# Performance work log

Hardware: AMD Instinct MI355X
Metric: run time of the kernel (lower is better)

Reference implementation:

```python
import jax, jax.numpy as jnp
import numpy as np

NUM_HEADS = 16
EPS = 1e-6
ROPE_BASE = 10000.0

def _thw(N, TT):
    table = {2640: (3, 22, 40), 1530: (3, 17, 30), 6120: (3, 34, 60), 660: (3, 11, 20)}
    return table.get(N - TT, (3, 23, 40))

def _positions(t, h, w):
    tt, hh, ww = np.meshgrid(np.arange(t), np.arange(h), np.arange(w), indexing='ij')
    return jnp.asarray(np.stack([tt, hh, ww], -1).reshape(-1, 3), jnp.float32)  # (THW, 3)

def _rope1d(x, pos):
    # x: (B,H,T,d) one axis-chunk, pos: (T,) positions for that axis
    d = x.shape[-1]
    inv_freq = 1.0 / (ROPE_BASE ** (jnp.arange(0, d, 2, dtype=jnp.float32) / d))
    ang = pos[:, None] * inv_freq                     # (T, d/2)
    cos = jnp.concatenate([jnp.cos(ang)] * 2, -1)     # (T, d)
    sin = jnp.concatenate([jnp.sin(ang)] * 2, -1)
    x1, x2 = x[..., : d // 2], x[..., d // 2:]
    return x * cos + jnp.concatenate([-x2, x1], -1) * sin

def _rope3d(x, pos, TT):
    # first TT tokens (text) pass through; video tokens get per-axis rotation
    pre, vid = x[:, :, :TT], x[:, :, TT:]
    chunks = jnp.split(vid, 3, axis=-1)               # t/h/w axis chunks
    rot = [_rope1d(c, pos[:, i]) for i, c in enumerate(chunks)]
    return jnp.concatenate([pre, jnp.concatenate(rot, -1)], axis=2)

def _rms(x, w):
    return x * jax.lax.rsqrt(jnp.mean(x * x, -1, keepdims=True) + EPS) * w

def setup_inputs() -> dict:
    key = jax.random.key(0)
    ks = jax.random.split(key, 12)
    B, N, C = 1, 2866, 1536
    Dh = C // NUM_HEADS
    s = 0.02
    return {
        'x': jax.random.normal(ks[0], (B, N, C), jnp.float32),
        'Wq': jax.random.normal(ks[1], (C, C), jnp.float32) * s,
        'bq': jnp.zeros((C,), jnp.float32),
        'Wk': jax.random.normal(ks[2], (C, C), jnp.float32) * s,
        'bk': jnp.zeros((C,), jnp.float32),
        'Wv': jax.random.normal(ks[3], (C, C), jnp.float32) * s,
        'bv': jnp.zeros((C,), jnp.float32),
        'qn_w': jnp.ones((Dh,), jnp.float32),
        'kn_w': jnp.ones((Dh,), jnp.float32),
        'Wp': jax.random.normal(ks[4], (C, C), jnp.float32) * s,
        'bp': jnp.zeros((C,), jnp.float32),
        'TT': 226,
    }

def reference(x, Wq, bq, Wk, bk, Wv, bv, qn_w, kn_w, Wp, bp, TT):
    B, N, C = x.shape
    H = NUM_HEADS
    Dh = C // H
    def proj(W, b):
        return (x @ W.T + b).reshape(B, N, H, Dh).transpose(0, 2, 1, 3)  # (B,H,N,Dh)
    q, k, v = proj(Wq, bq), proj(Wk, bk), proj(Wv, bv)
    q, k = _rms(q, qn_w), _rms(k, kn_w)
    t, h, w = _thw(N, TT)
    pos = _positions(t, h, w)
    q = _rope3d(q, pos, TT)
    k = _rope3d(k, pos, TT)
    scale = Dh ** -0.5
    attn = jax.nn.softmax(jnp.einsum('bhqd,bhkd->bhqk', q, k) * scale, axis=-1)
    o = jnp.einsum('bhqk,bhkd->bhqd', attn, v)
    o = o.transpose(0, 2, 1, 3).reshape(B, N, C)
    return o @ Wp.T + bp
```

## Files before the change

kernel.cpp:

```cpp
#include <hip/hip_runtime.h>
#include <hip/hip_bf16.h>
#include <math.h>

#define C_DIM 1536
#define H_NUM 16
#define DH    96

typedef __attribute__((ext_vector_type(4))) float  f32x4;
typedef __attribute__((ext_vector_type(8))) short  bf16x8;

__device__ __forceinline__ unsigned short f2bf_rne(float f) {
    unsigned u = __float_as_uint(f);
    unsigned r = (u + 0x7FFFu + ((u >> 16) & 1u)) >> 16;
    return (unsigned short)r;
}
__device__ __forceinline__ float bf2f(unsigned short h) {
    return __uint_as_float(((unsigned)h) << 16);
}

__device__ __forceinline__ void glds16(const void* g, void* l) {
    __builtin_amdgcn_global_load_lds(
        (const __attribute__((address_space(1))) unsigned int*)g,
        (__attribute__((address_space(3))) unsigned int*)l, 16, 0, 0);
}

__global__ __launch_bounds__(256)
void cvt_split(const float* __restrict__ in, unsigned short* __restrict__ hi,
               unsigned short* __restrict__ lo, int n4)
{
    const int i = blockIdx.x * 256 + threadIdx.x;
    if (i >= n4) return;
    float4 v = *(const float4*)&in[4 * i];
    unsigned short h[4], l[4];
    float vv[4] = {v.x, v.y, v.z, v.w};
    #pragma unroll
    for (int j = 0; j < 4; ++j) {
        h[j] = f2bf_rne(vv[j]);
        l[j] = f2bf_rne(vv[j] - bf2f(h[j]));
    }
    *(ushort4*)&hi[4 * i] = *(ushort4*)h;
    *(ushort4*)&lo[4 * i] = *(ushort4*)l;
}

struct CvtArgs {
    const float* src[4];
    unsigned short* hi[4];
    unsigned short* lo[4];
};
__global__ __launch_bounds__(256)
void cvt_split4(CvtArgs a, int n4)
{
    const int i = blockIdx.x * 256 + threadIdx.x;
    if (i >= n4) return;
    const int w = blockIdx.y;
    float4 v = *(const float4*)&a.src[w][4 * i];
    unsigned short h[4], l[4];
    float vv[4] = {v.x, v.y, v.z, v.w};
    #pragma unroll
    for (int j = 0; j < 4; ++j) {
        h[j] = f2bf_rne(vv[j]);
        l[j] = f2bf_rne(vv[j] - bf2f(h[j]));
    }
    *(ushort4*)&a.hi[w][4 * i] = *(ushort4*)h;
    *(ushort4*)&a.lo[w][4 * i] = *(ushort4*)l;
}

__global__ __launch_bounds__(256)
void gemm_mfma(const unsigned short* __restrict__ Ahi,
               const unsigned short* __restrict__ Alo,
               const unsigned short* W0h, const unsigned short* W0l,
               const float* b0, float* Y0,
               const unsigned short* W1h, const unsigned short* W1l,
               const float* b1, float* Y1,
               const unsigned short* W2h, const unsigned short* W2l,
               const float* b2, float* Y2,
               int M)
{
    __shared__ __align__(16) unsigned short lds[2 * 4 * 4096];

    const unsigned short* Wh;
    const unsigned short* Wl;
    const float* bias;
    float* Y;
    if (blockIdx.z == 0)      { Wh = W0h; Wl = W0l; bias = b0; Y = Y0; }
    else if (blockIdx.z == 1) { Wh = W1h; Wl = W1l; bias = b1; Y = Y1; }
    else                      { Wh = W2h; Wl = W2l; bias = b2; Y = Y2; }

    const int t   = threadIdx.x;
    const int m0  = blockIdx.x * 128;
    const int n0  = blockIdx.y * 128;
    const int w   = t >> 6;
    const int l   = t & 63;

    const unsigned short* src =
        (w == 0) ? Ahi : (w == 1) ? Alo : (w == 2) ? Wh : Wl;
    const int rbase = (w < 2) ? m0 : n0;
    const int rmax  = (w < 2) ? (M - 1) : 0x3FFFFFFF;
    const int srow  = l >> 2;
    const int scol  = l & 3;
    const int ssw   = (srow >> 1) & 3;
    int goff[8];
    #pragma unroll
    for (int i = 0; i < 8; ++i) {
        int gr = rbase + 16 * i + srow;
        gr = gr < rmax ? gr : rmax;
        goff[i] = gr * C_DIM + 8 * (scol ^ ssw);
    }

    const int lane = t & 63;
    const int wv   = t >> 6;
    const int wm   = wv & 1, wn = wv >> 1;
    const int lrow = lane & 15;
    const int quad = lane >> 4;
    const int pc   = quad ^ ((lrow >> 1) & 3);
    int aoff[4], boff[4];
    #pragma unroll
    for (int i = 0; i < 4; ++i) {
        aoff[i] = (64 * wm + 16 * i + lrow) * 32 + 8 * pc;
        boff[i] = (64 * wn + 16 * i + lrow) * 32 + 8 * pc;
    }

    f32x4 acc[4][4];
    #pragma unroll
    for (int i = 0; i < 4; ++i)
        #pragma unroll
        for (int j = 0; j < 4; ++j) acc[i][j] = (f32x4)0.f;

    #pragma unroll
    for (int i = 0; i < 8; ++i)
        glds16(src + goff[i], (char*)&lds[w * 4096] + i * 1024);

    const int NT = C_DIM / 32;
    for (int kt = 0; kt < NT; ++kt) {
        const int cb = kt & 1;
        const unsigned short* sA = lds + cb * 16384;

        asm volatile("s_waitcnt vmcnt(0)" ::: "memory");
        __builtin_amdgcn_s_barrier();
        __builtin_amdgcn_sched_barrier(0);

        bf16x8 ah[2], al[2], bh[4], bl[4];

        if (kt + 1 < NT) {
            char* dN = (char*)&lds[(cb ^ 1) * 16384 + w * 4096];
            const int k0n = (kt + 1) * 32;
            #pragma unroll
            for (int i = 0; i < 8; ++i)
                glds16(src + goff[i] + k0n, dN + i * 1024);
        }
        #pragma unroll
        for (int j = 0; j < 4; ++j) {
            bh[j] = *(const bf16x8*)&sA[8192 + boff[j]];
            bl[j] = *(const bf16x8*)&sA[12288 + boff[j]];
        }
        #pragma unroll
        for (int i = 0; i < 2; ++i) {
            ah[i] = *(const bf16x8*)&sA[aoff[i]];
            al[i] = *(const bf16x8*)&sA[4096 + aoff[i]];
        }
        __builtin_amdgcn_s_barrier();
        asm volatile("s_waitcnt lgkmcnt(0)" ::: "memory");
        __builtin_amdgcn_sched_barrier(0);
        __builtin_amdgcn_s_setprio(1);
        #pragma unroll
        for (int i = 0; i < 2; ++i)
            #pragma unroll
            for (int j = 0; j < 4; ++j) {
                acc[i][j] = __builtin_amdgcn_mfma_f32_16x16x32_bf16(ah[i], bh[j], acc[i][j], 0, 0, 0);
                acc[i][j] = __builtin_amdgcn_mfma_f32_16x16x32_bf16(al[i], bh[j], acc[i][j], 0, 0, 0);
                acc[i][j] = __builtin_amdgcn_mfma_f32_16x16x32_bf16(ah[i], bl[j], acc[i][j], 0, 0, 0);
            }
        __builtin_amdgcn_s_setprio(0);
        __builtin_amdgcn_s_barrier();
        __builtin_amdgcn_sched_barrier(0);

        #pragma unroll
        for (int i = 0; i < 2; ++i) {
            ah[i] = *(const bf16x8*)&sA[aoff[2 + i]];
            al[i] = *(const bf16x8*)&sA[4096 + aoff[2 + i]];
        }
        __builtin_amdgcn_s_barrier();
        asm volatile("s_waitcnt lgkmcnt(0)" ::: "memory");
        __builtin_amdgcn_sched_barrier(0);
        __builtin_amdgcn_s_setprio(1);
        #pragma unroll
        for (int i = 0; i < 2; ++i)
            #pragma unroll
            for (int j = 0; j < 4; ++j) {
                acc[2 + i][j] = __builtin_amdgcn_mfma_f32_16x16x32_bf16(ah[i], bh[j], acc[2 + i][j], 0, 0, 0);
                acc[2 + i][j] = __builtin_amdgcn_mfma_f32_16x16x32_bf16(al[i], bh[j], acc[2 + i][j], 0, 0, 0);
                acc[2 + i][j] = __builtin_amdgcn_mfma_f32_16x16x32_bf16(ah[i], bl[j], acc[2 + i][j], 0, 0, 0);
            }
        __builtin_amdgcn_s_setprio(0);
    }

    float bv[4];
    #pragma unroll
    for (int j = 0; j < 4; ++j) bv[j] = bias[n0 + 64 * wn + 16 * j + lrow];
    #pragma unroll
    for (int i = 0; i < 4; ++i) {
        const int rbase2 = m0 + 64 * wm + 16 * i + 4 * quad;
        #pragma unroll
        for (int p = 0; p < 4; ++p) {
            const int row = rbase2 + p;
            if (row >= M) continue;
            #pragma unroll
            for (int j = 0; j < 4; ++j) {
                const int col = n0 + 64 * wn + 16 * j + lrow;
                Y[(size_t)row * C_DIM + col] = acc[i][j][p] + bv[j];
            }
        }
    }
}

__global__ __launch_bounds__(512, 2)
void gemm_mfma256(const unsigned short* __restrict__ Ahi,
                  const unsigned short* __restrict__ Alo,
                  const unsigned short* W0h, const unsigned short* W0l,
                  const float* b0, float* Y0,
                  const unsigned short* W1h, const unsigned short* W1l,
                  const float* b1, float* Y1,
                  const unsigned short* W2h, const unsigned short* W2l,
                  const float* b2, float* Y2,
                  int M)
{
    extern __shared__ __align__(16) unsigned short smem[];

    const unsigned short* Wh;
    const unsigned short* Wl;
    const float* bias;
    float* Y;
    if (blockIdx.z == 0)      { Wh = W0h; Wl = W0l; bias = b0; Y = Y0; }
    else if (blockIdx.z == 1) { Wh = W1h; Wl = W1l; bias = b1; Y = Y1; }
    else                      { Wh = W2h; Wl = W2l; bias = b2; Y = Y2; }

    const int t    = threadIdx.x;
    const int wv   = t >> 6;
    const int lane = t & 63;
    const int m0   = blockIdx.x * 256;
    const int n0   = blockIdx.y * 256;

    const int mat  = wv >> 1;
    const int half = wv & 1;
    const unsigned short* src =
        (mat == 0) ? Ahi : (mat == 1) ? Alo : (mat == 2) ? Wh : Wl;
    const int rbase = (mat < 2) ? m0 : n0;
    const int rmax  = (mat < 2) ? (M - 1) : 0x3FFFFFFF;
    const int srow  = lane >> 2;
    const int scol  = lane & 3;
    const int ssw   = (srow >> 1) & 3;
    int goff[8];
    #pragma unroll
    for (int i = 0; i < 8; ++i) {
        int gr = rbase + half * 128 + 16 * i + srow;
        gr = gr < rmax ? gr : rmax;
        goff[i] = gr * C_DIM + 8 * (scol ^ ssw);
    }
    unsigned short* const dstBase = smem + mat * 8192 + half * 4096;

    const int wm   = wv & 1;
    const int wn   = wv >> 1;
    const int lrow = lane & 15;
    const int quad = lane >> 4;
    const int pc   = quad ^ ((lrow >> 1) & 3);
    int aoff[8], boff[4];
    #pragma unroll
    for (int i = 0; i < 8; ++i)
        aoff[i] = (128 * wm + 16 * i + lrow) * 32 + 8 * pc;
    #pragma unroll
    for (int j = 0; j < 4; ++j)
        boff[j] = (64 * wn + 16 * j + lrow) * 32 + 8 * pc;

    f32x4 acc[8][4];
    #pragma unroll
    for (int i = 0; i < 8; ++i)
        #pragma unroll
        for (int j = 0; j < 4; ++j) acc[i][j] = (f32x4)0.f;

    #pragma unroll
    for (int i = 0; i < 8; ++i)
        glds16(src + goff[i], (char*)dstBase + i * 1024);

    const int NT = C_DIM / 32;
    for (int kt = 0; kt < NT; ++kt) {
        const int cb = kt & 1;
        const unsigned short* sA = smem + cb * 32768;
        unsigned short* dN = dstBase + (cb ^ 1) * 32768;
        const int k0n = (kt + 1) * 32;
        const bool pf = (kt + 1 < NT);

        asm volatile("s_waitcnt vmcnt(0)" ::: "memory");
        __builtin_amdgcn_s_barrier();
        __builtin_amdgcn_sched_barrier(0);

        bf16x8 bh[4], bl[4], ah[2], al[2];

        if (pf) {
            #pragma unroll
            for (int i = 0; i < 8; ++i)
                glds16(src + goff[i] + k0n, (char*)dN + i * 1024);
        }
        #pragma unroll
        for (int j = 0; j < 4; ++j) {
            bh[j] = *(const bf16x8*)&sA[16384 + boff[j]];
            bl[j] = *(const bf16x8*)&sA[24576 + boff[j]];
        }
        #pragma unroll
        for (int i = 0; i < 2; ++i) {
            ah[i] = *(const bf16x8*)&sA[aoff[i]];
            al[i] = *(const bf16x8*)&sA[8192 + aoff[i]];
        }
        __builtin_amdgcn_s_barrier();
        asm volatile("s_waitcnt lgkmcnt(0)" ::: "memory");
        __builtin_amdgcn_sched_barrier(0);
        __builtin_amdgcn_s_setprio(1);
        #pragma unroll
        for (int i = 0; i < 2; ++i)
            #pragma unroll
            for (int j = 0; j < 4; ++j) {
                acc[i][j] = __builtin_amdgcn_mfma_f32_16x16x32_bf16(ah[i], bh[j], acc[i][j], 0, 0, 0);
                acc[i][j] = __builtin_amdgcn_mfma_f32_16x16x32_bf16(al[i], bh[j], acc[i][j], 0, 0, 0);
                acc[i][j] = __builtin_amdgcn_mfma_f32_16x16x32_bf16(ah[i], bl[j], acc[i][j], 0, 0, 0);
            }
        __builtin_amdgcn_s_setprio(0);
        __builtin_amdgcn_s_barrier();
        __builtin_amdgcn_sched_barrier(0);

        #pragma unroll
        for (int i = 0; i < 2; ++i) {
            ah[i] = *(const bf16x8*)&sA[aoff[2 + i]];
            al[i] = *(const bf16x8*)&sA[8192 + aoff[2 + i]];
        }
        __builtin_amdgcn_s_barrier();
        asm volatile("s_waitcnt lgkmcnt(0)" ::: "memory");
        __builtin_amdgcn_sched_barrier(0);
        __builtin_amdgcn_s_setprio(1);
        #pragma unroll
        for (int i = 0; i < 2; ++i)
            #pragma unroll
            for (int j = 0; j < 4; ++j) {
                acc[2 + i][j] = __builtin_amdgcn_mfma_f32_16x16x32_bf16(ah[i], bh[j], acc[2 + i][j], 0, 0, 0);
                acc[2 + i][j] = __builtin_amdgcn_mfma_f32_16x16x32_bf16(al[i], bh[j], acc[2 + i][j], 0, 0, 0);
                acc[2 + i][j] = __builtin_amdgcn_mfma_f32_16x16x32_bf16(ah[i], bl[j], acc[2 + i][j], 0, 0, 0);
            }
        __builtin_amdgcn_s_setprio(0);
        __builtin_amdgcn_s_barrier();
        __builtin_amdgcn_sched_barrier(0);

        #pragma unroll
        for (int i = 0; i < 2; ++i) {
            ah[i] = *(const bf16x8*)&sA[aoff[4 + i]];
            al[i] = *(const bf16x8*)&sA[8192 + aoff[4 + i]];
        }
        __builtin_amdgcn_s_barrier();
        asm volatile("s_waitcnt lgkmcnt(0)" ::: "memory");
        __builtin_amdgcn_sched_barrier(0);
        __builtin_amdgcn_s_setprio(1);
        #pragma unroll
        for (int i = 0; i < 2; ++i)
            #pragma unroll
            for (int j = 0; j < 4; ++j) {
                acc[4 + i][j] = __builtin_amdgcn_mfma_f32_16x16x32_bf16(ah[i], bh[j], acc[4 + i][j], 0, 0, 0);
                acc[4 + i][j] = __builtin_amdgcn_mfma_f32_16x16x32_bf16(al[i], bh[j], acc[4 + i][j], 0, 0, 0);
                acc[4 + i][j] = __builtin_amdgcn_mfma_f32_16x16x32_bf16(ah[i], bl[j], acc[4 + i][j], 0, 0, 0);
            }
        __builtin_amdgcn_s_setprio(0);
        __builtin_amdgcn_s_barrier();
        __builtin_amdgcn_sched_barrier(0);

        #pragma unroll
        for (int i = 0; i < 2; ++i) {
            ah[i] = *(const bf16x8*)&sA[aoff[6 + i]];
            al[i] = *(const bf16x8*)&sA[8192 + aoff[6 + i]];
        }
        __builtin_amdgcn_s_barrier();
        asm volatile("s_waitcnt lgkmcnt(0)" ::: "memory");
        __builtin_amdgcn_sched_barrier(0);
        __builtin_amdgcn_s_setprio(1);
        #pragma unroll
        for (int i = 0; i < 2; ++i)
            #pragma unroll
            for (int j = 0; j < 4; ++j) {
                acc[6 + i][j] = __builtin_amdgcn_mfma_f32_16x16x32_bf16(ah[i], bh[j], acc[6 + i][j], 0, 0, 0);
                acc[6 + i][j] = __builtin_amdgcn_mfma_f32_16x16x32_bf16(al[i], bh[j], acc[6 + i][j], 0, 0, 0);
                acc[6 + i][j] = __builtin_amdgcn_mfma_f32_16x16x32_bf16(ah[i], bl[j], acc[6 + i][j], 0, 0, 0);
            }
        __builtin_amdgcn_s_setprio(0);
    }

    float bv2[4];
    #pragma unroll
    for (int j = 0; j < 4; ++j) bv2[j] = bias[n0 + 64 * wn + 16 * j + lrow];
    #pragma unroll
    for (int i = 0; i < 8; ++i) {
        const int rbase2 = m0 + 128 * wm + 16 * i + 4 * quad;
        #pragma unroll
        for (int p = 0; p < 4; ++p) {
            const int row = rbase2 + p;
            if (row >= M) continue;
            #pragma unroll
            for (int j = 0; j < 4; ++j) {
                const int col = n0 + 64 * wn + 16 * j + lrow;
                Y[(size_t)row * C_DIM + col] = acc[i][j][p] + bv2[j];
            }
        }
    }
}

__global__ __launch_bounds__(256)
void rms_rope_split(const float* __restrict__ q, const float* __restrict__ k,
                    const float* __restrict__ qw, const float* __restrict__ kw,
                    const int* __restrict__ TTp,
                    unsigned short* __restrict__ qhi,
                    unsigned short* __restrict__ khi, int Ntok)
{
    const int idx = blockIdx.x * 256 + threadIdx.x;
    if (idx >= Ntok * H_NUM) return;
    const int h = idx & (H_NUM - 1);
    const int n = idx >> 4;

    const float* src;
    const float* w;
    if (blockIdx.y == 0) { src = q; w = qw; } else { src = k; w = kw; }
    const float* p = src + (size_t)n * C_DIM + h * DH;

    float x[DH];
    #pragma unroll
    for (int i = 0; i < DH / 4; ++i) *(float4*)&x[4 * i] = *(const float4*)&p[4 * i];

    float ss = 0.f;
    #pragma unroll
    for (int i = 0; i < DH; ++i) ss += x[i] * x[i];
    const float r = rsqrtf(ss * (1.0f / DH) + 1e-6f);
    #pragma unroll
    for (int i = 0; i < DH; ++i) x[i] *= r * w[i];

    const int TT = *TTp;
    if (n >= TT) {
        const int pidx = n - TT;
        const int NT = Ntok - TT;
        int hh = 23, ww = 40;
        if      (NT == 2640) { hh = 22; ww = 40; }
        else if (NT == 1530) { hh = 17; ww = 30; }
        else if (NT == 6120) { hh = 34; ww = 60; }
        else if (NT ==  660) { hh = 11; ww = 20; }
        float pos[3];
        pos[0] = (float)(pidx / (hh * ww));
        pos[1] = (float)((pidx / ww) % hh);
        pos[2] = (float)(pidx % ww);
        #pragma unroll
        for (int c = 0; c < 3; ++c) {
            #pragma unroll
            for (int j = 0; j < 16; ++j) {
                const float invf = exp2f(-0.83048202373f * (float)j);
                const float ang  = pos[c] * invf;
                const float cs = cosf(ang), sn = sinf(ang);
                const float a = x[32 * c + j], b = x[32 * c + j + 16];
                x[32 * c + j]      = a * cs - b * sn;
                x[32 * c + j + 16] = a * sn + b * cs;
            }
        }
    }

    const size_t off = (size_t)n * C_DIM + h * DH;
    const float qscale = 0.14724445f;
    if (blockIdx.y == 0) {
        #pragma unroll
        for (int i = 0; i < DH / 4; ++i) {
            unsigned short hb[4];
            #pragma unroll
            for (int j = 0; j < 4; ++j) hb[j] = f2bf_rne(x[4 * i + j] * qscale);
            *(ushort4*)&qhi[off + 4 * i] = *(ushort4*)hb;
        }
    } else {
        #pragma unroll
        for (int i = 0; i < DH / 4; ++i) {
            unsigned short hb[4];
            #pragma unroll
            for (int j = 0; j < 4; ++j) hb[j] = f2bf_rne(x[4 * i + j]);
            *(ushort4*)&khi[off + 4 * i] = *(ushort4*)hb;
        }
    }
}

__global__ __launch_bounds__(256)
void transpose_v(const float* __restrict__ V, unsigned short* __restrict__ vt,
                 int Ntok, int vtStride)
{
    __shared__ unsigned short tile[96 * 72];
    const int t  = threadIdx.x;
    const int k0 = blockIdx.x * 64;
    const int h  = blockIdx.y;

    #pragma unroll
    for (int it = 0; it < 6; ++it) {
        const int idx = t + 256 * it;
        const int key = idx / 24, dg = idx % 24;
        float vv[4] = {0.f, 0.f, 0.f, 0.f};
        if (k0 + key < Ntok)
            *(float4*)vv = *(const float4*)&V[(size_t)(k0 + key) * C_DIM + h * DH + 4 * dg];
        #pragma unroll
        for (int j = 0; j < 4; ++j) tile[(4 * dg + j) * 72 + key] = f2bf_rne(vv[j]);
    }
    __syncthreads();
    #pragma unroll
    for (int it = 0; it < 3; ++it) {
        const int idx = t + 256 * it;
        const int d = idx >> 3, ck = idx & 7;
        *(bf16x8*)&vt[((size_t)h * DH + d) * vtStride + k0 + 8 * ck] =
            *(const bf16x8*)&tile[d * 72 + 8 * ck];
    }
}

__global__ __launch_bounds__(256)
void attn_mfma(const unsigned short* __restrict__ qhi,
               const unsigned short* __restrict__ khi,
               const unsigned short* __restrict__ vt,
               unsigned short* __restrict__ Ohi,
               unsigned short* __restrict__ Olo,
               int Ntok, int nKt, int vtStride)
{
    __shared__ unsigned short ldsK[64 * 96];
    __shared__ unsigned short ldsV[96 * 72];
    __shared__ unsigned short ldsP[64 * 72];
    __shared__ float ldsL[64];

    const int t    = threadIdx.x;
    const int lane = t & 63;
    const int wv   = t >> 6;
    const int lrow = lane & 15;
    const int quad = lane >> 4;

    const int Lb  = blockIdx.x + gridDim.x * blockIdx.y;
    const int xcd = Lb & 7;
    const int jj  = Lb >> 3;
    const int h   = 2 * xcd + (jj >= nKt ? 1 : 0);
    const int q0  = (jj >= nKt ? jj - nKt : jj) * 64;
    const size_t hoff = (size_t)h * DH;

    bf16x8 qh[3];
    {
        const int qr = q0 + wv * 16 + lrow;
        if (qr < Ntok) {
            const size_t base = (size_t)qr * C_DIM + hoff + quad * 8;
            #pragma unroll
            for (int kc = 0; kc < 3; ++kc)
                qh[kc] = *(const bf16x8*)&qhi[base + 32 * kc];
        } else {
            const bf16x8 z = {0,0,0,0,0,0,0,0};
            #pragma unroll
            for (int kc = 0; kc < 3; ++kc) qh[kc] = z;
        }
    }

    const int rK  = t >> 2;
    const int cK  = t & 3;
    const int swK = (rK >> 1) & 3;
    const int swf = (lrow >> 1) & 3;
    const int vd  = t >> 3;
    const int vck = t & 7;

    float lsum = 0.f;
    f32x4 oacc[6];
    #pragma unroll
    for (int dt = 0; dt < 6; ++dt) oacc[dt] = (f32x4)0.f;

    const bf16x8 zv = {0,0,0,0,0,0,0,0};
    bf16x8 pk[3], pv[3];
    #pragma unroll
    for (int it = 0; it < 3; ++it) {
        pk[it] = (rK < Ntok) ? *(const bf16x8*)&khi[(size_t)rK * C_DIM + hoff + 8 * (cK + 4 * it)] : zv;
        pv[it] = *(const bf16x8*)&vt[(hoff + vd + 32 * it) * vtStride + 8 * vck];
    }

    const int pRow = (wv * 16 + lrow) * 72;
    for (int kt = 0; kt < nKt; ++kt) {
        const int k0 = kt * 64;
        __syncthreads();
        #pragma unroll
        for (int it = 0; it < 3; ++it) {
            *(bf16x8*)&ldsK[rK * 96 + 8 * (4 * it + (cK ^ swK))] = pk[it];
            *(bf16x8*)&ldsV[(vd + 32 * it) * 72 + 8 * vck]       = pv[it];
        }
        __syncthreads();

        if (kt + 1 < nKt) {
            const int kn = k0 + 64;
            #pragma unroll
            for (int it = 0; it < 3; ++it) {
                pk[it] = (kn + rK < Ntok) ? *(const bf16x8*)&khi[(size_t)(kn + rK) * C_DIM + hoff + 8 * (cK + 4 * it)] : zv;
                pv[it] = *(const bf16x8*)&vt[(hoff + vd + 32 * it) * vtStride + kn + 8 * vck];
            }
        }

        f32x4 sacc[4];
        #pragma unroll
        for (int mt = 0; mt < 4; ++mt) sacc[mt] = (f32x4)0.f;
        #pragma unroll
        for (int kc = 0; kc < 3; ++kc) {
            #pragma unroll
            for (int mt = 0; mt < 4; ++mt) {
                bf16x8 kb = *(const bf16x8*)&ldsK[(lrow + 16 * mt) * 96 + 8 * (4 * kc + (quad ^ swf))];
                sacc[mt] = __builtin_amdgcn_mfma_f32_16x16x32_bf16(kb, qh[kc], sacc[mt], 0, 0, 0);
            }
        }

        if (kt + 1 < nKt) {
            #pragma unroll
            for (int mt = 0; mt < 4; ++mt) {
                float e[4];
                #pragma unroll
                for (int p = 0; p < 4; ++p) e[p] = exp2f(sacc[mt][p]);
                lsum += (e[0] + e[1]) + (e[2] + e[3]);
                unsigned u0 = __float_as_uint(e[0]) + 0x8000u;
                unsigned u1 = __float_as_uint(e[1]) + 0x8000u;
                unsigned u2 = __float_as_uint(e[2]) + 0x8000u;
                unsigned u3 = __float_as_uint(e[3]) + 0x8000u;
                uint2 pr;
                pr.x = __builtin_amdgcn_perm(u1, u0, 0x07060302u);
                pr.y = __builtin_amdgcn_perm(u3, u2, 0x07060302u);
                *(uint2*)&ldsP[pRow + 16 * mt + 4 * quad] = pr;
            }
        } else {
            const int kq = k0 + 4 * quad;
            #pragma unroll
            for (int mt = 0; mt < 4; ++mt) {
                float e[4];
                #pragma unroll
                for (int p = 0; p < 4; ++p)
                    e[p] = (kq + 16 * mt + p < Ntok) ? exp2f(sacc[mt][p]) : 0.f;
                lsum += (e[0] + e[1]) + (e[2] + e[3]);
                unsigned u0 = __float_as_uint(e[0]) + 0x8000u;
                unsigned u1 = __float_as_uint(e[1]) + 0x8000u;
                unsigned u2 = __float_as_uint(e[2]) + 0x8000u;
                unsigned u3 = __float_as_uint(e[3]) + 0x8000u;
                uint2 pr;
                pr.x = __builtin_amdgcn_perm(u1, u0, 0x07060302u);
                pr.y = __builtin_amdgcn_perm(u3, u2, 0x07060302u);
                *(uint2*)&ldsP[pRow + 16 * mt + 4 * quad] = pr;
            }
        }

        #pragma unroll
        for (int kc2 = 0; kc2 < 2; ++kc2) {
            bf16x8 pa = *(const bf16x8*)&ldsP[pRow + 32 * kc2 + 8 * quad];
            #pragma unroll
            for (int dt = 0; dt < 6; ++dt) {
                bf16x8 vb = *(const bf16x8*)&ldsV[(16 * dt + lrow) * 72 + 32 * kc2 + 8 * quad];
                oacc[dt] = __builtin_amdgcn_mfma_f32_16x16x32_bf16(pa, vb, oacc[dt], 0, 0, 0);
            }
        }
    }

    lsum += __shfl_xor(lsum, 16, 64);
    lsum += __shfl_xor(lsum, 32, 64);
    ldsL[wv * 16 + lrow] = lsum;
    #pragma unroll
    for (int p = 0; p < 4; ++p) {
        const int row = q0 + wv * 16 + quad * 4 + p;
        if (row >= Ntok) continue;
        const float rl = 1.0f / ldsL[wv * 16 + quad * 4 + p];
        const size_t rbase = (size_t)row * C_DIM + hoff + lrow;
        #pragma unroll
        for (int dt = 0; dt < 6; ++dt) {
            const float o = oacc[dt][p] * rl;
            const unsigned short hb = f2bf_rne(o);
            Ohi[rbase + 16 * dt] = hb;
            Olo[rbase + 16 * dt] = f2bf_rne(o - bf2f(hb));
        }
    }
}

extern "C" void kernel_launch(void* const* d_in, const int* in_sizes, int n_in,
                              void* d_out, int out_size, void* d_ws, size_t ws_size,
                              hipStream_t stream)
{
    const float* x   = (const float*)d_in[0];
    const float* Wq  = (const float*)d_in[1];
    const float* bq  = (const float*)d_in[2];
    const float* Wk  = (const float*)d_in[3];
    const float* bk  = (const float*)d_in[4];
    const float* Wv  = (const float*)d_in[5];
    const float* bv  = (const float*)d_in[6];
    const float* qnw = (const float*)d_in[7];
    const float* knw = (const float*)d_in[8];
    const float* Wp  = (const float*)d_in[9];
    const float* bp  = (const float*)d_in[10];
    const int*   TTp = (const int*)d_in[11];

    const int Ntok = in_sizes[0] / C_DIM;
    const int nKt  = (Ntok + 63) / 64;
    const int vtStride = nKt * 64;
    const size_t NC = (size_t)Ntok * C_DIM;
    const size_t CC = (size_t)C_DIM * C_DIM;
    float* out = (float*)d_out;

    static bool s_attr = false;
    if (!s_attr) {
        hipFuncSetAttribute(reinterpret_cast<const void*>(gemm_mfma256),
                            hipFuncAttributeMaxDynamicSharedMemorySize, 131072);
        s_attr = true;
    }

    float*          kbuf = (float*)d_ws;
    float*          vbuf = kbuf + NC;
    unsigned short* xhi  = (unsigned short*)(vbuf + NC);
    unsigned short* xlo  = xhi + NC;
    unsigned short* wsp  = xlo + NC;
    unsigned short* wqh = wsp + 0 * CC, *wql = wsp + 1 * CC;
    unsigned short* wkh = wsp + 2 * CC, *wkl = wsp + 3 * CC;
    unsigned short* wvh = wsp + 4 * CC, *wvl = wsp + 5 * CC;
    unsigned short* wph = wsp + 6 * CC, *wpl = wsp + 7 * CC;
    unsigned short* qhib = wsp + 8 * CC;
    unsigned short* khib = qhib + NC;
    unsigned short* vtb  = khib + NC;
    float*          qbuf = out;
    unsigned short* ohi  = (unsigned short*)kbuf;
    unsigned short* olo  = ohi + NC;

    cvt_split<<<dim3((NC / 4 + 255) / 256), 256, 0, stream>>>(x, xhi, xlo, (int)(NC / 4));
    CvtArgs ca;
    ca.src[0] = Wq; ca.hi[0] = wqh; ca.lo[0] = wql;
    ca.src[1] = Wk; ca.hi[1] = wkh; ca.lo[1] = wkl;
    ca.src[2] = Wv; ca.hi[2] = wvh; ca.lo[2] = wvl;
    ca.src[3] = Wp; ca.hi[3] = wph; ca.lo[3] = wpl;
    cvt_split4<<<dim3((CC / 4 + 255) / 256, 4), 256, 0, stream>>>(ca, (int)(CC / 4));

    dim3 qkvgrid((Ntok + 255) / 256, C_DIM / 256, 3);
    gemm_mfma256<<<qkvgrid, 512, 131072, stream>>>(xhi, xlo,
        wqh, wql, bq, qbuf,
        wkh, wkl, bk, kbuf,
        wvh, wvl, bv, vbuf, Ntok);

    const int nv = Ntok * H_NUM;
    rms_rope_split<<<dim3((nv + 255) / 256, 2), 256, 0, stream>>>(
        qbuf, kbuf, qnw, knw, TTp, qhib, khib, Ntok);

    transpose_v<<<dim3(nKt, H_NUM), 256, 0, stream>>>(vbuf, vtb, Ntok, vtStride);

    attn_mfma<<<dim3(nKt, H_NUM), 256, 0, stream>>>(
        qhib, khib, vtb, ohi, olo, Ntok, nKt, vtStride);

    dim3 pgrid((Ntok + 127) / 128, C_DIM / 128, 1);
    gemm_mfma<<<pgrid, 256, 0, stream>>>(ohi, olo,
        wph, wpl, bp, out,
        wph, wpl, bp, out,
        wph, wpl, bp, out, Ntok);
}
```

Before: 485.4 us.

## Process 128 query rows per attention block and split GEMM prefetch issue

The attention kernel now gives each wave two 16-row query groups, so a block covers 128 queries and every K/V tile staged in LDS is reused across twice as many rows. The grid shrinks to half as many query blocks per head. This halves K/V global loads and LDS staging per query, but raises register pressure and may reduce occupancy and parallelism. Separately, the QKV GEMM's next-tile global-to-LDS prefetch is split into two halves issued at different points in the k-loop to spread memory traffic between the MFMA phases.

Result: no change. 488.5 us (+0.6%).

```diff
diff --git a/kernel.cpp b/kernel.cpp
--- a/kernel.cpp
+++ b/kernel.cpp
@@ -297,7 +297,7 @@
 
         if (pf) {
             #pragma unroll
-            for (int i = 0; i < 8; ++i)
+            for (int i = 0; i < 4; ++i)
                 glds16(src + goff[i] + k0n, (char*)dN + i * 1024);
         }
         #pragma unroll
@@ -326,6 +326,11 @@
         __builtin_amdgcn_s_barrier();
         __builtin_amdgcn_sched_barrier(0);
 
+        if (pf) {
+            #pragma unroll
+            for (int i = 4; i < 8; ++i)
+                glds16(src + goff[i] + k0n, (char*)dN + i * 1024);
+        }
         #pragma unroll
         for (int i = 0; i < 2; ++i) {
             ah[i] = *(const bf16x8*)&sA[aoff[2 + i]];
@@ -522,8 +527,8 @@
 {
     __shared__ unsigned short ldsK[64 * 96];
     __shared__ unsigned short ldsV[96 * 72];
-    __shared__ unsigned short ldsP[64 * 72];
-    __shared__ float ldsL[64];
+    __shared__ unsigned short ldsP[128 * 72];
+    __shared__ float ldsL[128];
 
     const int t    = threadIdx.x;
     const int lane = t & 63;
@@ -531,25 +536,27 @@
     const int lrow = lane & 15;
     const int quad = lane >> 4;
 
-    const int Lb  = blockIdx.x + gridDim.x * blockIdx.y;
+    const int nQb = gridDim.x;
+    const int Lb  = blockIdx.x + nQb * blockIdx.y;
     const int xcd = Lb & 7;
     const int jj  = Lb >> 3;
-    const int h   = 2 * xcd + (jj >= nKt ? 1 : 0);
-    const int q0  = (jj >= nKt ? jj - nKt : jj) * 64;
+    const int h   = 2 * xcd + (jj >= nQb ? 1 : 0);
+    const int q0  = (jj >= nQb ? jj - nQb : jj) * 128;
     const size_t hoff = (size_t)h * DH;
 
-    bf16x8 qh[3];
-    {
-        const int qr = q0 + wv * 16 + lrow;
+    bf16x8 qh[2][3];
+    #pragma unroll
+    for (int qg = 0; qg < 2; ++qg) {
+        const int qr = q0 + wv * 32 + qg * 16 + lrow;
         if (qr < Ntok) {
             const size_t base = (size_t)qr * C_DIM + hoff + quad * 8;
             #pragma unroll
             for (int kc = 0; kc < 3; ++kc)
-                qh[kc] = *(const bf16x8*)&qhi[base + 32 * kc];
+                qh[qg][kc] = *(const bf16x8*)&qhi[base + 32 * kc];
         } else {
             const bf16x8 z = {0,0,0,0,0,0,0,0};
             #pragma unroll
-            for (int kc = 0; kc < 3; ++kc) qh[kc] = z;
+            for (int kc = 0; kc < 3; ++kc) qh[qg][kc] = z;
         }
     }
 
@@ -560,10 +567,12 @@
     const int vd  = t >> 3;
     const int vck = t & 7;
 
-    float lsum = 0.f;
-    f32x4 oacc[6];
-    #pragma unroll
-    for (int dt = 0; dt < 6; ++dt) oacc[dt] = (f32x4)0.f;
+    float lsum[2] = {0.f, 0.f};
+    f32x4 oacc[2][6];
+    #pragma unroll
+    for (int qg = 0; qg < 2; ++qg)
+        #pragma unroll
+        for (int dt = 0; dt < 6; ++dt) oacc[qg][dt] = (f32x4)0.f;
 
     const bf16x8 zv = {0,0,0,0,0,0,0,0};
     bf16x8 pk[3], pv[3];
@@ -573,7 +582,8 @@
         pv[it] = *(const bf16x8*)&vt[(hoff + vd + 32 * it) * vtStride + 8 * vck];
     }
 
-    const int pRow = (wv * 16 + lrow) * 72;
+    const int pRow0 = (wv * 32 + lrow) * 72;
+    const int pRow1 = pRow0 + 16 * 72;
     for (int kt = 0; kt < nKt; ++kt) {
         const int k0 = kt * 64;
         __syncthreads();
@@ -593,80 +603,99 @@
             }
         }
 
-        f32x4 sacc[4];
-        #pragma unroll
-        for (int mt = 0; mt < 4; ++mt) sacc[mt] = (f32x4)0.f;
+        f32x4 sacc[2][4];
+        #pragma unroll
+        for (int qg = 0; qg < 2; ++qg)
+            #pragma unroll
+            for (int mt = 0; mt < 4; ++mt) sacc[qg][mt] = (f32x4)0.f;
         #pragma unroll
         for (int kc = 0; kc < 3; ++kc) {
             #pragma unroll
             for (int mt = 0; mt < 4; ++mt) {
                 bf16x8 kb = *(const bf16x8*)&ldsK[(lrow + 16 * mt) * 96 + 8 * (4 * kc + (quad ^ swf))];
-                sacc[mt] = __builtin_amdgcn_mfma_f32_16x16x32_bf16(kb, qh[kc], sacc[mt], 0, 0, 0);
+                sacc[0][mt] = __builtin_amdgcn_mfma_f32_16x16x32_bf16(kb, qh[0][kc], sacc[0][mt], 0, 0, 0);
+                sacc[1][mt] = __builtin_amdgcn_mfma_f32_16x16x32_bf16(kb, qh[1][kc], sacc[1][mt], 0, 0, 0);
             }
         }
 
         if (kt + 1 < nKt) {
             #pragma unroll
-            for (int mt = 0; mt < 4; ++mt) {
-                float e[4];
+            for (int qg = 0; qg < 2; ++qg) {
+                const int pR = qg ? pRow1 : pRow0;
                 #pragma unroll
-                for (int p = 0; p < 4; ++p) e[p] = exp2f(sacc[mt][p]);
-                lsum += (e[0] + e[1]) + (e[2] + e[3]);
-                unsigned u0 = __float_as_uint(e[0]) + 0x8000u;
-                unsigned u1 = __float_as_uint(e[1]) + 0x8000u;
-                unsigned u2 = __float_as_uint(e[2]) + 0x8000u;
-                unsigned u3 = __float_as_uint(e[3]) + 0x8000u;
-                uint2 pr;
-                pr.x = __builtin_amdgcn_perm(u1, u0, 0x07060302u);
-                pr.y = __builtin_amdgcn_perm(u3, u2, 0x07060302u);
-                *(uint2*)&ldsP[pRow + 16 * mt + 4 * quad] = pr;
+                for (int mt = 0; mt < 4; ++mt) {
+                    float e[4];
+                    #pragma unroll
+                    for (int p = 0; p < 4; ++p) e[p] = exp2f(sacc[qg][mt][p]);
+                    lsum[qg] += (e[0] + e[1]) + (e[2] + e[3]);
+                    unsigned u0 = __float_as_uint(e[0]) + 0x8000u;
+                    unsigned u1 = __float_as_uint(e[1]) + 0x8000u;
+                    unsigned u2 = __float_as_uint(e[2]) + 0x8000u;
+                    unsigned u3 = __float_as_uint(e[3]) + 0x8000u;
+                    uint2 pr;
+                    pr.x = __builtin_amdgcn_perm(u1, u0, 0x07060302u);
+                    pr.y = __builtin_amdgcn_perm(u3, u2, 0x07060302u);
+                    *(uint2*)&ldsP[pR + 16 * mt + 4 * quad] = pr;
+                }
             }
         } else {
             const int kq = k0 + 4 * quad;
             #pragma unroll
-            for (int mt = 0; mt < 4; ++mt) {
-                float e[4];
+            for (int qg = 0; qg < 2; ++qg) {
+                const int pR = qg ? pRow1 : pRow0;
                 #pragma unroll
-                for (int p = 0; p < 4; ++p)
-                    e[p] = (kq + 16 * mt + p < Ntok) ? exp2f(sacc[mt][p]) : 0.f;
-                lsum += (e[0] + e[1]) + (e[2] + e[3]);
-                unsigned u0 = __float_as_uint(e[0]) + 0x8000u;
-                unsigned u1 = __float_as_uint(e[1]) + 0x8000u;
-                unsigned u2 = __float_as_uint(e[2]) + 0x8000u;
-                unsigned u3 = __float_as_uint(e[3]) + 0x8000u;
-                uint2 pr;
-                pr.x = __builtin_amdgcn_perm(u1, u0, 0x07060302u);
-                pr.y = __builtin_amdgcn_perm(u3, u2, 0x07060302u);
-                *(uint2*)&ldsP[pRow + 16 * mt + 4 * quad] = pr;
+                for (int mt = 0; mt < 4; ++mt) {
+                    float e[4];
+                    #pragma unroll
+                    for (int p = 0; p < 4; ++p)
+                        e[p] = (kq + 16 * mt + p < Ntok) ? exp2f(sacc[qg][mt][p]) : 0.f;
+                    lsum[qg] += (e[0] + e[1]) + (e[2] + e[3]);
+                    unsigned u0 = __float_as_uint(e[0]) + 0x8000u;
+                    unsigned u1 = __float_as_uint(e[1]) + 0x8000u;
+                    unsigned u2 = __float_as_uint(e[2]) + 0x8000u;
+                    unsigned u3 = __float_as_uint(e[3]) + 0x8000u;
+                    uint2 pr;
+                    pr.x = __builtin_amdgcn_perm(u1, u0, 0x07060302u);
+                    pr.y = __builtin_amdgcn_perm(u3, u2, 0x07060302u);
+                    *(uint2*)&ldsP[pR + 16 * mt + 4 * quad] = pr;
+                }
             }
         }
 
         #pragma unroll
         for (int kc2 = 0; kc2 < 2; ++kc2) {
-            bf16x8 pa = *(const bf16x8*)&ldsP[pRow + 32 * kc2 + 8 * quad];
+            bf16x8 pa0 = *(const bf16x8*)&ldsP[pRow0 + 32 * kc2 + 8 * quad];
+            bf16x8 pa1 = *(const bf16x8*)&ldsP[pRow1 + 32 * kc2 + 8 * quad];
             #pragma unroll
             for (int dt = 0; dt < 6; ++dt) {
                 bf16x8 vb = *(const bf16x8*)&ldsV[(16 * dt + lrow) * 72 + 32 * kc2 + 8 * quad];
-                oacc[dt] = __builtin_amdgcn_mfma_f32_16x16x32_bf16(pa, vb, oacc[dt], 0, 0, 0);
-            }
-        }
-    }
-
-    lsum += __shfl_xor(lsum, 16, 64);
-    lsum += __shfl_xor(lsum, 32, 64);
-    ldsL[wv * 16 + lrow] = lsum;
-    #pragma unroll
-    for (int p = 0; p < 4; ++p) {
-        const int row = q0 + wv * 16 + quad * 4 + p;
-        if (row >= Ntok) continue;
-        const float rl = 1.0f / ldsL[wv * 16 + quad * 4 + p];
-        const size_t rbase = (size_t)row * C_DIM + hoff + lrow;
-        #pragma unroll
-        for (int dt = 0; dt < 6; ++dt) {
-            const float o = oacc[dt][p] * rl;
-            const unsigned short hb = f2bf_rne(o);
-            Ohi[rbase + 16 * dt] = hb;
-            Olo[rbase + 16 * dt] = f2bf_rne(o - bf2f(hb));
+                oacc[0][dt] = __builtin_amdgcn_mfma_f32_16x16x32_bf16(pa0, vb, oacc[0][dt], 0, 0, 0);
+                oacc[1][dt] = __builtin_amdgcn_mfma_f32_16x16x32_bf16(pa1, vb, oacc[1][dt], 0, 0, 0);
+            }
+        }
+    }
+
+    #pragma unroll
+    for (int qg = 0; qg < 2; ++qg) {
+        lsum[qg] += __shfl_xor(lsum[qg], 16, 64);
+        lsum[qg] += __shfl_xor(lsum[qg], 32, 64);
+        ldsL[wv * 32 + qg * 16 + lrow] = lsum[qg];
+    }
+    #pragma unroll
+    for (int qg = 0; qg < 2; ++qg) {
+        #pragma unroll
+        for (int p = 0; p < 4; ++p) {
+            const int row = q0 + wv * 32 + qg * 16 + quad * 4 + p;
+            if (row >= Ntok) continue;
+            const float rl = 1.0f / ldsL[wv * 32 + qg * 16 + quad * 4 + p];
+            const size_t rbase = (size_t)row * C_DIM + hoff + lrow;
+            #pragma unroll
+            for (int dt = 0; dt < 6; ++dt) {
+                const float o = oacc[qg][dt][p] * rl;
+                const unsigned short hb = f2bf_rne(o);
+                Ohi[rbase + 16 * dt] = hb;
+                Olo[rbase + 16 * dt] = f2bf_rne(o - bf2f(hb));
+            }
         }
     }
 }
@@ -690,6 +719,7 @@
 
     const int Ntok = in_sizes[0] / C_DIM;
     const int nKt  = (Ntok + 63) / 64;
+    const int nQb  = (Ntok + 127) / 128;
     const int vtStride = nKt * 64;
     const size_t NC = (size_t)Ntok * C_DIM;
     const size_t CC = (size_t)C_DIM * C_DIM;
@@ -738,7 +768,7 @@
 
     transpose_v<<<dim3(nKt, H_NUM), 256, 0, stream>>>(vbuf, vtb, Ntok, vtStride);
 
-    attn_mfma<<<dim3(nKt, H_NUM), 256, 0, stream>>>(
+    attn_mfma<<<dim3(nQb, H_NUM), 256, 0, stream>>>(
         qhib, khib, vtb, ohi, olo, Ntok, nKt, vtStride);
 
     dim3 pgrid((Ntok + 127) / 128, C_DIM / 128, 1);
```
